# Performance work log

Measured on AMD Instinct MI355X. Metric: run time of the kernel, lower is better.

## Reference

```python
import jax, jax.numpy as jnp
import numpy as np

D_MODEL = 2048
HQ = 32          # query heads
HKV = 8          # kv heads
HD = D_MODEL // HQ   # head_dim = 64
G = HQ // HKV        # group size = 4
THETA = 10000.0


def _rope(x, pos):
    """x: (B, H, T, D), pos: (B, T) int. Rotates even/odd interleaved pairs."""
    D = x.shape[-1]
    inv_freq = THETA ** (-jnp.arange(0, D, 2, dtype=jnp.float32) / D)   # (D/2,)
    ang = pos[:, None, :, None].astype(jnp.float32) * inv_freq          # (B,1,T,D/2)
    cos, sin = jnp.cos(ang), jnp.sin(ang)
    x1, x2 = x[..., 0::2], x[..., 1::2]
    r1 = x1 * cos - x2 * sin
    r2 = x1 * sin + x2 * cos
    return jnp.stack([r1, r2], axis=-1).reshape(x.shape)


def setup_inputs() -> dict:
    key = jax.random.key(0)
    ks = jax.random.split(key, 5)
    B, T = 2, 2048
    s = lambda fan_in: 1.0 / np.sqrt(fan_in)
    return {
        "x": jax.random.normal(ks[0], (B, T, D_MODEL), jnp.float32),
        "token_positions": jnp.arange(T, dtype=jnp.int32),
        "WQ": jax.random.normal(ks[1], (HQ * HD, D_MODEL), jnp.float32) * s(D_MODEL),
        "WK": jax.random.normal(ks[2], (HKV * HD, D_MODEL), jnp.float32) * s(D_MODEL),
        "WV": jax.random.normal(ks[3], (HKV * HD, D_MODEL), jnp.float32) * s(D_MODEL),
        "WO": jax.random.normal(ks[4], (D_MODEL, HQ * HD), jnp.float32) * s(HQ * HD),
    }


def reference(x, token_positions, WQ, WK, WV, WO):
    B, T, _ = x.shape
    pos = token_positions if token_positions.ndim == 2 else jnp.broadcast_to(token_positions[None, :], (B, T))

    # Projections (Linear is y = x @ W.T, no bias)
    Q = (x @ WQ.T).reshape(B, T, HQ, HD).transpose(0, 2, 1, 3)    # (B,Hq,T,D)
    K = (x @ WK.T).reshape(B, T, HKV, HD).transpose(0, 2, 1, 3)   # (B,Hkv,T,D)
    V = (x @ WV.T).reshape(B, T, HKV, HD).transpose(0, 2, 1, 3)

    Q = _rope(Q, pos)
    K = _rope(K, pos)

    # GQA: group query heads per kv head instead of duplicating K/V
    Qg = Q.reshape(B, HKV, G, T, HD)
    scale = jnp.float32(1.0 / np.sqrt(HD))
    scores = jnp.einsum('bkgqd,bkld->bkgql', Qg, K) * scale       # (B,Hkv,G,T,T)

    causal = jnp.tril(jnp.ones((T, T), dtype=bool))
    scores = jnp.where(causal, scores, jnp.finfo(scores.dtype).min)
    A = jax.nn.softmax(scores, axis=-1)

    O = jnp.einsum('bkgql,bkld->bkgqd', A, V)                     # (B,Hkv,G,T,D)
    O = O.reshape(B, HQ, T, HD).transpose(0, 2, 1, 3).reshape(B, T, HQ * HD)
    return O @ WO.T
```

## Files before the change

### kernel.cpp

```cpp
#include <hip/hip_runtime.h>
#include <hip/hip_bf16.h>

#define B_   2
#define T_   2048
#define DM_  2048
#define HQ_  32
#define HKV_ 8
#define HD_  64

typedef __attribute__((ext_vector_type(8))) short bf16x8;
typedef __attribute__((ext_vector_type(4))) float f32x4;
typedef __fp16 f16x4 __attribute__((ext_vector_type(4)));
typedef __fp16 f16x2 __attribute__((ext_vector_type(2)));

__device__ __forceinline__ unsigned short f2bf(float f) {
    unsigned int u = __float_as_uint(f);
    u = (u + 0x7fffu + ((u >> 16) & 1u)) >> 16;
    return (unsigned short)u;
}

__device__ __forceinline__ void gload16(const unsigned short* g, unsigned short* l) {
    __builtin_amdgcn_global_load_lds(
        (const __attribute__((address_space(1))) unsigned int*)g,
        (__attribute__((address_space(3))) unsigned int*)l, 16, 0, 0);
}


__global__ __launch_bounds__(256) void convert_all(
    const float* __restrict__ x,  const float* __restrict__ WQ,
    const float* __restrict__ WK, const float* __restrict__ WV,
    const float* __restrict__ WO, unsigned short* __restrict__ ws)
{
    int i = blockIdx.x*256 + threadIdx.x;
    const float* src; unsigned short* dst; int rel;
    if (i < 2097152)      { src = x;  dst = ws;                 rel = i; }
    else if (i < 3145728) { src = WQ; dst = ws + 8388608;       rel = i - 2097152; }
    else if (i < 3407872) { src = WK; dst = ws + 8388608+4194304; rel = i - 3145728; }
    else if (i < 3670016) { src = WV; dst = ws + 8388608+5242880; rel = i - 3407872; }
    else                  { src = WO; dst = ws + 14680064;      rel = i - 3670016; }
    float4 v = *(const float4*)(src + (size_t)rel*4);
    uint2 pk;
    pk.x = (unsigned int)f2bf(v.x) | ((unsigned int)f2bf(v.y) << 16);
    pk.y = (unsigned int)f2bf(v.z) | ((unsigned int)f2bf(v.w) << 16);
    *(uint2*)(dst + (size_t)rel*4) = pk;
}

__global__ __launch_bounds__(256) void qkv_gemm_bf16(
    const unsigned short* __restrict__ Ab, const unsigned short* __restrict__ Wb,
    unsigned short* __restrict__ Qb, unsigned short* __restrict__ Kb,
    unsigned short* __restrict__ Vt)
{
    __shared__ unsigned short As[3][128*32];
    __shared__ unsigned short Bs[3][128*32];
    const int tid  = threadIdx.x;
    const int ln   = tid & 63;
    const int wv   = tid >> 6;
    const int wm   = (wv >> 1) * 64;
    const int wn   = (wv & 1) * 64;
    const int col  = ln & 15;
    const int quad = ln >> 4;

    const int bid = blockIdx.x;
    const int swz = (bid & 7) * 96 + (bid >> 3);
    const int n0  = (swz % 24) * 128;
    const int m0  = (swz / 24) * 128;

    const int cg = ((tid & 3) ^ ((tid >> 3) & 3)) * 8;
    const unsigned short* aG = Ab + (size_t)(m0 + (tid>>2))*DM_ + cg;
    const unsigned short* bG = Wb + (size_t)(n0 + (tid>>2))*DM_ + cg;
    const int ck = (quad ^ ((col >> 1) & 3)) * 8;

    f32x4 acc[4][4];
    #pragma unroll
    for (int i=0;i<4;++i)
        #pragma unroll
        for (int j=0;j<4;++j) { acc[i][j][0]=0.f; acc[i][j][1]=0.f; acc[i][j][2]=0.f; acc[i][j][3]=0.f; }

    auto stage = [&](int buf, int k0) {
        unsigned short* aL = &As[buf][wv*512];
        unsigned short* bL = &Bs[buf][wv*512];
        gload16(aG + k0,                  aL);
        gload16(aG + (size_t)64*DM_ + k0, aL + 2048);
        gload16(bG + k0,                  bL);
        gload16(bG + (size_t)64*DM_ + k0, bL + 2048);
    };

    stage(0, 0);
    stage(1, 32);

    int kt = 0;
    for (int k0 = 0; k0 < DM_; k0 += 32, ++kt) {
        if (k0 + 32 < DM_) {
            asm volatile("s_waitcnt vmcnt(4)" ::: "memory");
        } else {
            asm volatile("s_waitcnt vmcnt(0)" ::: "memory");
        }
        __builtin_amdgcn_s_barrier();
        if (k0 + 64 < DM_) stage((kt+2)%3, k0 + 64);
        const unsigned short* Ac = As[kt%3];
        const unsigned short* Bc = Bs[kt%3];
        bf16x8 af[4], bfr[4];
        #pragma unroll
        for (int i=0;i<4;++i) {
            af[i]  = *(const bf16x8*)&Ac[(wm + i*16 + col)*32 + ck];
            bfr[i] = *(const bf16x8*)&Bc[(wn + i*16 + col)*32 + ck];
        }
        #pragma unroll
        for (int i=0;i<4;++i)
            #pragma unroll
            for (int j=0;j<4;++j)
                acc[i][j] = __builtin_amdgcn_mfma_f32_16x16x32_bf16(af[i], bfr[j], acc[i][j], 0, 0, 0);
    }

    const int b  = m0 >> 11;
    const int tb = m0 & 2047;
    #pragma unroll
    for (int j=0;j<4;++j) {
        const int n = n0 + wn + j*16 + col;
        #pragma unroll
        for (int i=0;i<4;++i) {
            const int t = tb + wm + i*16 + quad*4;
            if (n < 2048) {
                #pragma unroll
                for (int r=0;r<4;++r)
                    Qb[(((size_t)(b*HQ_ + (n>>6)))*T_ + t + r)*HD_ + (n&63)] = f2bf(acc[i][j][r]);
            } else if (n < 2560) {
                #pragma unroll
                for (int r=0;r<4;++r)
                    Kb[(((size_t)(b*HKV_ + ((n-2048)>>6)))*T_ + t + r)*HD_ + (n&63)] = f2bf(acc[i][j][r]);
            } else {
                unsigned short* vp = Vt + (((size_t)(b*HKV_ + ((n-2560)>>6)))*HD_ + (n&63))*T_ + t;
                union { f16x2 h; unsigned int u; } c0, c1;
                c0.h = __builtin_amdgcn_cvt_pkrtz(acc[i][j][0], acc[i][j][1]);
                c1.h = __builtin_amdgcn_cvt_pkrtz(acc[i][j][2], acc[i][j][3]);
                *(unsigned int*)(vp)     = c0.u;
                *(unsigned int*)(vp + 2) = c1.u;
            }
        }
    }
}

__global__ __launch_bounds__(256) void rope_inplace(
    unsigned short* __restrict__ Qb, unsigned short* __restrict__ Kb,
    const int* __restrict__ pos)
{
    const int NQ = B_*HQ_*T_*(HD_/2);
    const int NK = B_*HKV_*T_*(HD_/2);
    int idx = blockIdx.x*256 + threadIdx.x;
    unsigned short* base; float scale;
    int rem;
    if (idx < NQ) { base = Qb; rem = idx; scale = 0.18033688011112042f; }
    else { rem = idx - NQ; if (rem >= NK) return; base = Kb; scale = 1.0f; }
    const int i  = rem & 31;
    const int t  = (rem >> 5) & (T_ - 1);
    const int bh = rem >> 16;
    size_t off = (((size_t)bh)*T_ + t)*HD_ + (i<<1);
    unsigned int pk = *(unsigned int*)(base + off);
    float x1 = __uint_as_float((pk & 0xffffu) << 16);
    float x2 = __uint_as_float(pk & 0xffff0000u);
    float p = (float)pos[t];
    float inv = exp2f(-13.287712379549449f * ((float)(i<<1)) * (1.0f/64.0f));
    float ang = p * inv;
    float sn, cs;
    sincosf(ang, &sn, &cs);
    float r1 = (x1*cs - x2*sn) * scale;
    float r2 = (x1*sn + x2*cs) * scale;
    unsigned int out = (unsigned int)f2bf(r1) | ((unsigned int)f2bf(r2) << 16);
    *(unsigned int*)(base + off) = out;
}

__global__ __launch_bounds__(256, 2) void attn_mfma(
    const unsigned short* __restrict__ Qb, const unsigned short* __restrict__ Kb,
    const unsigned short* __restrict__ Vh, unsigned short* __restrict__ Ob)
{
    __shared__ unsigned short Ks[2][64*64];
    __shared__ unsigned short Vs[2][64*64];

    const int tid  = threadIdx.x;
    const int lane = tid & 63;
    const int wave = tid >> 6;
    const int q16  = lane & 15;
    const int quad = lane >> 4;
    const int bxi  = blockIdx.x;
    const int bh   = blockIdx.y;
    const int b    = bh >> 5;
    const int h    = bh & 31;
    const int kvh  = h >> 2;
    const int qa   = bxi;
    const int qbt  = 31 - bxi;
    const int qgA  = qa *64 + wave*16 + q16;
    const int qgB  = qbt*64 + wave*16 + q16;

    const unsigned short* kbase = Kb + ((size_t)(b*HKV_ + kvh))*T_*HD_;
    const unsigned short* vbase = Vh + ((size_t)(b*HKV_ + kvh))*(size_t)HD_*T_;

    const bf16x8 qA0 = *(const bf16x8*)(Qb + ((size_t)bh*T_ + qgA)*HD_ + quad*8);
    const bf16x8 qA1 = *(const bf16x8*)(Qb + ((size_t)bh*T_ + qgA)*HD_ + 32 + quad*8);
    const bf16x8 qB0 = *(const bf16x8*)(Qb + ((size_t)bh*T_ + qgB)*HD_ + quad*8);
    const bf16x8 qB1 = *(const bf16x8*)(Qb + ((size_t)bh*T_ + qgB)*HD_ + 32 + quad*8);

    f32x4 oA[4], oB[4];
    #pragma unroll
    for (int i=0;i<4;++i) {
        oA[i][0]=0.f; oA[i][1]=0.f; oA[i][2]=0.f; oA[i][3]=0.f;
        oB[i][0]=0.f; oB[i][1]=0.f; oB[i][2]=0.f; oB[i][3]=0.f;
    }
    float lA = 0.f, lB = 0.f;

    const int sr = tid >> 3;
    const int sj = tid & 7;
    const int sc = (sj ^ (sr & 7)) * 8;

    const int rk7 = q16 & 7;
    const int ck0 = (quad ^ rk7) * 8;
    const int ck1 = ((quad + 4) ^ rk7) * 8;

    auto smrow = [&](const f32x4 s, float& ps) -> f16x4 {
        float e0 = exp2f(s[0]), e1 = exp2f(s[1]);
        float e2 = exp2f(s[2]), e3 = exp2f(s[3]);
        ps += (e0+e1) + (e2+e3);
        union { f16x2 h[2]; f16x4 v; } c;
        c.h[0] = __builtin_amdgcn_cvt_pkrtz(e0, e1);
        c.h[1] = __builtin_amdgcn_cvt_pkrtz(e2, e3);
        return c.v;
    };

    uint4 kr0, kr1, vr0, vr1;
    kr0 = *(const uint4*)(kbase + (size_t)sr*HD_ + sj*8);
    kr1 = *(const uint4*)(kbase + (size_t)(sr+32)*HD_ + sj*8);
    vr0 = *(const uint4*)(vbase + (size_t)sr*T_ + sj*8);
    vr1 = *(const uint4*)(vbase + (size_t)(sr+32)*T_ + sj*8);
    *(uint4*)&Ks[0][sr*64 + sc]      = kr0;
    *(uint4*)&Ks[0][(sr+32)*64 + sc] = kr1;
    *(uint4*)&Vs[0][sr*64 + sc]      = vr0;
    *(uint4*)&Vs[0][(sr+32)*64 + sc] = vr1;
    kr0 = *(const uint4*)(kbase + (size_t)(64+sr)*HD_ + sj*8);
    kr1 = *(const uint4*)(kbase + (size_t)(64+sr+32)*HD_ + sj*8);
    vr0 = *(const uint4*)(vbase + (size_t)sr*T_ + 64 + sj*8);
    vr1 = *(const uint4*)(vbase + (size_t)(sr+32)*T_ + 64 + sj*8);
    __syncthreads();

    int cur = 0;

    for (int kt = 0; kt <= qa; ++kt) {
        const unsigned short* KsC = Ks[cur];
        const unsigned short* VsC = Vs[cur];
        const int nxt = cur ^ 1;

        f32x4 sB[4], sA[4];
        #pragma unroll
        for (int t=0;t<4;++t) {
            sB[t][0]=0.f; sB[t][1]=0.f; sB[t][2]=0.f; sB[t][3]=0.f;
            sA[t][0]=0.f; sA[t][1]=0.f; sA[t][2]=0.f; sA[t][3]=0.f;
        }
        f16x4 pfB[4];
        float psB = 0.f, psA = 0.f;

        __builtin_amdgcn_s_setprio(1);
        #pragma unroll
        for (int t = 0; t < 4; ++t) {
            const int rk = (t*16 + q16) * 64;
            bf16x8 a0 = *(const bf16x8*)&KsC[rk + ck0];
            bf16x8 a1 = *(const bf16x8*)&KsC[rk + ck1];
            sB[t] = __builtin_amdgcn_mfma_f32_16x16x32_bf16(a0, qB0, sB[t], 0, 0, 0);
            sB[t] = __builtin_amdgcn_mfma_f32_16x16x32_bf16(a1, qB1, sB[t], 0, 0, 0);
            sA[t] = __builtin_amdgcn_mfma_f32_16x16x32_bf16(a0, qA0, sA[t], 0, 0, 0);
            sA[t] = __builtin_amdgcn_mfma_f32_16x16x32_bf16(a1, qA1, sA[t], 0, 0, 0);
            if (t > 0) pfB[t-1] = smrow(sB[t-1], psB);
        }
        *(uint4*)&Ks[nxt][sr*64 + sc]      = kr0;
        *(uint4*)&Ks[nxt][(sr+32)*64 + sc] = kr1;
        *(uint4*)&Vs[nxt][sr*64 + sc]      = vr0;
        *(uint4*)&Vs[nxt][(sr+32)*64 + sc] = vr1;
        if (kt + 1 < qbt) {
            const int kn = (kt+2)*64;
            kr0 = *(const uint4*)(kbase + (size_t)(kn+sr)*HD_ + sj*8);
            kr1 = *(const uint4*)(kbase + (size_t)(kn+sr+32)*HD_ + sj*8);
            vr0 = *(const uint4*)(vbase + (size_t)sr*T_ + kn + sj*8);
            vr1 = *(const uint4*)(vbase + (size_t)(sr+32)*T_ + kn + sj*8);
        }
        pfB[3] = smrow(sB[3], psB);
        lB += psB;

        if (kt == qa) {
            #pragma unroll
            for (int t = 0; t < 4; ++t)
                #pragma unroll
                for (int r = 0; r < 4; ++r)
                    if (kt*64 + t*16 + quad*4 + r > qgA) sA[t][r] = -1e30f;
        }

        #pragma unroll
        for (int t = 0; t < 4; ++t) {
            const int cv = ((2*t + (quad>>1)) ^ rk7) * 8 + (quad&1)*4;
            f16x4 va[4];
            #pragma unroll
            for (int dt=0;dt<4;++dt)
                va[dt] = *(const f16x4*)&VsC[(dt*16 + q16)*64 + cv];
            #pragma unroll
            for (int dt=0;dt<4;++dt)
                oB[dt] = __builtin_amdgcn_mfma_f32_16x16x16f16(va[dt], pfB[t], oB[dt], 0, 0, 0);
            f16x4 pfA = smrow(sA[t], psA);
            #pragma unroll
            for (int dt=0;dt<4;++dt)
                oA[dt] = __builtin_amdgcn_mfma_f32_16x16x16f16(va[dt], pfA, oA[dt], 0, 0, 0);
        }
        lA += psA;
        __builtin_amdgcn_s_setprio(0);
        __syncthreads();
        cur ^= 1;
    }

    for (int kt = qa+1; kt <= qbt; ++kt) {
        const unsigned short* KsC = Ks[cur];
        const unsigned short* VsC = Vs[cur];
        const int nxt = cur ^ 1;

        f32x4 sB[4];
        #pragma unroll
        for (int t=0;t<4;++t) { sB[t][0]=0.f; sB[t][1]=0.f; sB[t][2]=0.f; sB[t][3]=0.f; }

        __builtin_amdgcn_s_setprio(1);
        #pragma unroll
        for (int t = 0; t < 4; ++t) {
            const int rk = (t*16 + q16) * 64;
            bf16x8 a0 = *(const bf16x8*)&KsC[rk + ck0];
            bf16x8 a1 = *(const bf16x8*)&KsC[rk + ck1];
            sB[t] = __builtin_amdgcn_mfma_f32_16x16x32_bf16(a0, qB0, sB[t], 0, 0, 0);
            sB[t] = __builtin_amdgcn_mfma_f32_16x16x32_bf16(a1, qB1, sB[t], 0, 0, 0);
        }
        if (kt < qbt) {
            *(uint4*)&Ks[nxt][sr*64 + sc]      = kr0;
            *(uint4*)&Ks[nxt][(sr+32)*64 + sc] = kr1;
            *(uint4*)&Vs[nxt][sr*64 + sc]      = vr0;
            *(uint4*)&Vs[nxt][(sr+32)*64 + sc] = vr1;
        }
        if (kt + 1 < qbt) {
            const int kn = (kt+2)*64;
            kr0 = *(const uint4*)(kbase + (size_t)(kn+sr)*HD_ + sj*8);
            kr1 = *(const uint4*)(kbase + (size_t)(kn+sr+32)*HD_ + sj*8);
            vr0 = *(const uint4*)(vbase + (size_t)sr*T_ + kn + sj*8);
            vr1 = *(const uint4*)(vbase + (size_t)(sr+32)*T_ + kn + sj*8);
        }
        if (kt == qbt) {
            #pragma unroll
            for (int t = 0; t < 4; ++t)
                #pragma unroll
                for (int r = 0; r < 4; ++r)
                    if (kt*64 + t*16 + quad*4 + r > qgB) sB[t][r] = -1e30f;
        }

        float psB = 0.f;
        #pragma unroll
        for (int t = 0; t < 4; ++t) {
            f16x4 pfB = smrow(sB[t], psB);
            const int cv = ((2*t + (quad>>1)) ^ rk7) * 8 + (quad&1)*4;
            #pragma unroll
            for (int dt=0;dt<4;++dt) {
                f16x4 va = *(const f16x4*)&VsC[(dt*16 + q16)*64 + cv];
                oB[dt] = __builtin_amdgcn_mfma_f32_16x16x16f16(va, pfB, oB[dt], 0, 0, 0);
            }
        }
        lB += psB;
        __builtin_amdgcn_s_setprio(0);
        __syncthreads();
        cur ^= 1;
    }

    lA += __shfl_xor(lA, 16); lA += __shfl_xor(lA, 32);
    lB += __shfl_xor(lB, 16); lB += __shfl_xor(lB, 32);
    const float rlA = 1.0f / lA;
    const float rlB = 1.0f / lB;
    unsigned short* opA = Ob + ((size_t)(b*T_ + qgA))*(HQ_*HD_) + h*HD_;
    unsigned short* opB = Ob + ((size_t)(b*T_ + qgB))*(HQ_*HD_) + h*HD_;
    #pragma unroll
    for (int dt = 0; dt < 4; ++dt) {
        uint2 pa, pb;
        pa.x = (unsigned int)f2bf(oA[dt][0]*rlA) | ((unsigned int)f2bf(oA[dt][1]*rlA) << 16);
        pa.y = (unsigned int)f2bf(oA[dt][2]*rlA) | ((unsigned int)f2bf(oA[dt][3]*rlA) << 16);
        pb.x = (unsigned int)f2bf(oB[dt][0]*rlB) | ((unsigned int)f2bf(oB[dt][1]*rlB) << 16);
        pb.y = (unsigned int)f2bf(oB[dt][2]*rlB) | ((unsigned int)f2bf(oB[dt][3]*rlB) << 16);
        *(uint2*)(opA + dt*16 + quad*4) = pa;
        *(uint2*)(opB + dt*16 + quad*4) = pb;
    }
}

__global__ __launch_bounds__(256) void out_gemm_bf16(
    const unsigned short* __restrict__ Ab, const unsigned short* __restrict__ Wb,
    float* __restrict__ C)
{
    __shared__ unsigned short As[3][128*32];
    __shared__ unsigned short Bs[3][128*32];
    const int tid  = threadIdx.x;
    const int ln   = tid & 63;
    const int wv   = tid >> 6;
    const int wm   = (wv >> 1) * 64;
    const int wn   = (wv & 1) * 64;
    const int col  = ln & 15;
    const int quad = ln >> 4;

    const int bid = blockIdx.x;
    const int swz = (bid & 7) * 64 + (bid >> 3);
    const int n0  = (swz & 15) * 128;
    const int m0  = (swz >> 4) * 128;

    const int cg = ((tid & 3) ^ ((tid >> 3) & 3)) * 8;
    const unsigned short* aG = Ab + (size_t)(m0 + (tid>>2))*DM_ + cg;
    const unsigned short* bG = Wb + (size_t)(n0 + (tid>>2))*DM_ + cg;
    const int ck = (quad ^ ((col >> 1) & 3)) * 8;

    f32x4 acc[4][4];
    #pragma unroll
    for (int i=0;i<4;++i)
        #pragma unroll
        for (int j=0;j<4;++j) { acc[i][j][0]=0.f; acc[i][j][1]=0.f; acc[i][j][2]=0.f; acc[i][j][3]=0.f; }

    auto stage = [&](int buf, int k0) {
        unsigned short* aL = &As[buf][wv*512];
        unsigned short* bL = &Bs[buf][wv*512];
        gload16(aG + k0,                  aL);
        gload16(aG + (size_t)64*DM_ + k0, aL + 2048);
        gload16(bG + k0,                  bL);
        gload16(bG + (size_t)64*DM_ + k0, bL + 2048);
    };

    stage(0, 0);
    stage(1, 32);

    int kt = 0;
    for (int k0 = 0; k0 < DM_; k0 += 32, ++kt) {
        if (k0 + 32 < DM_) {
            asm volatile("s_waitcnt vmcnt(4)" ::: "memory");
        } else {
            asm volatile("s_waitcnt vmcnt(0)" ::: "memory");
        }
        __builtin_amdgcn_s_barrier();
        if (k0 + 64 < DM_) stage((kt+2)%3, k0 + 64);
        const unsigned short* Ac = As[kt%3];
        const unsigned short* Bc = Bs[kt%3];
        bf16x8 af[4], bfr[4];
        #pragma unroll
        for (int i=0;i<4;++i) {
            af[i]  = *(const bf16x8*)&Ac[(wm + i*16 + col)*32 + ck];
            bfr[i] = *(const bf16x8*)&Bc[(wn + i*16 + col)*32 + ck];
        }
        #pragma unroll
        for (int i=0;i<4;++i)
            #pragma unroll
            for (int j=0;j<4;++j)
                acc[i][j] = __builtin_amdgcn_mfma_f32_16x16x32_bf16(af[i], bfr[j], acc[i][j], 0, 0, 0);
    }

    #pragma unroll
    for (int i=0;i<4;++i) {
        const int m = m0 + wm + i*16 + quad*4;
        #pragma unroll
        for (int j=0;j<4;++j) {
            const int n = n0 + wn + j*16 + col;
            #pragma unroll
            for (int r=0;r<4;++r)
                C[(size_t)(m + r)*DM_ + n] = acc[i][j][r];
        }
    }
}

extern "C" void kernel_launch(void* const* d_in, const int* in_sizes, int n_in,
                              void* d_out, int out_size, void* d_ws, size_t ws_size,
                              hipStream_t stream) {
    const float* x   = (const float*)d_in[0];
    const int*   pos = (const int*)  d_in[1];
    const float* WQ  = (const float*)d_in[2];
    const float* WK  = (const float*)d_in[3];
    const float* WV  = (const float*)d_in[4];
    const float* WO  = (const float*)d_in[5];
    float* out = (float*)d_out;

    unsigned short* xb  = (unsigned short*)d_ws;
    unsigned short* Wb  = xb  + (size_t)8388608;
    unsigned short* WOb = Wb  + (size_t)6291456;
    unsigned short* Qb  = WOb + (size_t)4194304;
    unsigned short* Kb  = Qb  + (size_t)8388608;
    unsigned short* Vt  = Kb  + (size_t)2097152;
    unsigned short* Ob  = Vt  + (size_t)2097152;

    convert_all<<<18432, 256, 0, stream>>>(x, WQ, WK, WV, WO, (unsigned short*)d_ws);

    qkv_gemm_bf16<<<768, 256, 0, stream>>>(xb, Wb, Qb, Kb, Vt);

    const int pairs = B_*HQ_*T_*(HD_/2) + B_*HKV_*T_*(HD_/2);
    rope_inplace<<<(pairs + 255)/256, 256, 0, stream>>>(Qb, Kb, pos);

    dim3 g3(16, B_*HQ_);
    attn_mfma<<<g3, 256, 0, stream>>>(Qb, Kb, Vt, Ob);

    out_gemm_bf16<<<512, 256, 0, stream>>>(Ob, WOb, out);
}
```

Measured before the change: 333.1 us.

## Fuse RoPE into QKV GEMM epilogue with precomputed trig table

```diff
diff --git a/kernel.cpp b/kernel.cpp
--- a/kernel.cpp
+++ b/kernel.cpp
@@ -26,12 +26,27 @@
 }
 
 
+#define CONV_N 4718592
+
 __global__ __launch_bounds__(256) void convert_all(
     const float* __restrict__ x,  const float* __restrict__ WQ,
     const float* __restrict__ WK, const float* __restrict__ WV,
-    const float* __restrict__ WO, unsigned short* __restrict__ ws)
+    const float* __restrict__ WO, unsigned short* __restrict__ ws,
+    const int* __restrict__ pos,  float* __restrict__ trig)
 {
     int i = blockIdx.x*256 + threadIdx.x;
+    if (i >= CONV_N) {
+        int j = i - CONV_N;
+        if (j < T_*32) {
+            int t = j >> 5, p = j & 31;
+            float inv = exp2f(-0.4152410118609203f * (float)p);
+            float ang = (float)pos[t] * inv;
+            float sn, cs;
+            sincosf(ang, &sn, &cs);
+            *(float2*)&trig[j*2] = make_float2(cs, sn);
+        }
+        return;
+    }
     const float* src; unsigned short* dst; int rel;
     if (i < 2097152)      { src = x;  dst = ws;                 rel = i; }
     else if (i < 3145728) { src = WQ; dst = ws + 8388608;       rel = i - 2097152; }
@@ -48,7 +63,7 @@
 __global__ __launch_bounds__(256) void qkv_gemm_bf16(
     const unsigned short* __restrict__ Ab, const unsigned short* __restrict__ Wb,
     unsigned short* __restrict__ Qb, unsigned short* __restrict__ Kb,
-    unsigned short* __restrict__ Vt)
+    unsigned short* __restrict__ Vt, const float* __restrict__ trig)
 {
     __shared__ unsigned short As[3][128*32];
     __shared__ unsigned short Bs[3][128*32];
@@ -85,50 +100,75 @@
         gload16(bG + (size_t)64*DM_ + k0, bL + 2048);
     };
 
+    auto kstep = [&](int bc, int k0v, int bstage, bool dostage, bool last) {
+        if (last) asm volatile("s_waitcnt vmcnt(0)" ::: "memory");
+        else      asm volatile("s_waitcnt vmcnt(4)" ::: "memory");
+        __builtin_amdgcn_s_barrier();
+        if (dostage) stage(bstage, k0v + 64);
+        const unsigned short* Ac = As[bc];
+        const unsigned short* Bc = Bs[bc];
+        bf16x8 af[4], bfr[4];
+        #pragma unroll
+        for (int i2=0;i2<4;++i2) {
+            af[i2]  = *(const bf16x8*)&Ac[(wm + i2*16 + col)*32 + ck];
+            bfr[i2] = *(const bf16x8*)&Bc[(wn + i2*16 + col)*32 + ck];
+        }
+        #pragma unroll
+        for (int i2=0;i2<4;++i2)
+            #pragma unroll
+            for (int j2=0;j2<4;++j2)
+                acc[i2][j2] = __builtin_amdgcn_mfma_f32_16x16x32_bf16(af[i2], bfr[j2], acc[i2][j2], 0, 0, 0);
+    };
+
     stage(0, 0);
     stage(1, 32);
 
-    int kt = 0;
-    for (int k0 = 0; k0 < DM_; k0 += 32, ++kt) {
-        if (k0 + 32 < DM_) {
-            asm volatile("s_waitcnt vmcnt(4)" ::: "memory");
-        } else {
-            asm volatile("s_waitcnt vmcnt(0)" ::: "memory");
-        }
-        __builtin_amdgcn_s_barrier();
-        if (k0 + 64 < DM_) stage((kt+2)%3, k0 + 64);
-        const unsigned short* Ac = As[kt%3];
-        const unsigned short* Bc = Bs[kt%3];
-        bf16x8 af[4], bfr[4];
-        #pragma unroll
-        for (int i=0;i<4;++i) {
-            af[i]  = *(const bf16x8*)&Ac[(wm + i*16 + col)*32 + ck];
-            bfr[i] = *(const bf16x8*)&Bc[(wn + i*16 + col)*32 + ck];
-        }
-        #pragma unroll
-        for (int i=0;i<4;++i)
-            #pragma unroll
-            for (int j=0;j<4;++j)
-                acc[i][j] = __builtin_amdgcn_mfma_f32_16x16x32_bf16(af[i], bfr[j], acc[i][j], 0, 0, 0);
-    }
+    int k0 = 0;
+    for (int rep = 0; rep < 20; ++rep) {
+        kstep(0, k0,      2, true, false);
+        kstep(1, k0+32,   0, true, false);
+        kstep(2, k0+64,   1, true, false);
+        k0 += 96;
+    }
+    kstep(0, 1920, 2, true,  false);
+    kstep(1, 1952, 0, true,  false);
+    kstep(2, 1984, 1, false, false);
+    kstep(0, 2016, 0, false, true);
 
     const int b  = m0 >> 11;
     const int tb = m0 & 2047;
     #pragma unroll
     for (int j=0;j<4;++j) {
         const int n = n0 + wn + j*16 + col;
-        #pragma unroll
-        for (int i=0;i<4;++i) {
-            const int t = tb + wm + i*16 + quad*4;
-            if (n < 2048) {
+        if (n < 2560) {
+            const int d   = n & 63;
+            const int p   = d >> 1;
+            const bool ev = (d & 1) == 0;
+            const float sc = (n < 2048) ? 0.18033688011112042f : 1.0f;
+            unsigned short* outp = (n < 2048)
+                ? Qb + (((size_t)(b*HQ_  + (n>>6)))*T_)*HD_
+                : Kb + (((size_t)(b*HKV_ + ((n-2048)>>6)))*T_)*HD_;
+            #pragma unroll
+            for (int i=0;i<4;++i) {
+                const int t0 = tb + wm + i*16 + quad*4;
                 #pragma unroll
-                for (int r=0;r<4;++r)
-                    Qb[(((size_t)(b*HQ_ + (n>>6)))*T_ + t + r)*HD_ + (n&63)] = f2bf(acc[i][j][r]);
-            } else if (n < 2560) {
-                #pragma unroll
-                for (int r=0;r<4;++r)
-                    Kb[(((size_t)(b*HKV_ + ((n-2048)>>6)))*T_ + t + r)*HD_ + (n&63)] = f2bf(acc[i][j][r]);
-            } else {
+                for (int r=0;r<4;++r) {
+                    float self = acc[i][j][r];
+                    float part = __shfl_xor(self, 1);
+                    float2 cs  = *(const float2*)&trig[((t0 + r)*32 + p)*2];
+                    float out  = ev ? (self*cs.x - part*cs.y)
+                                    : (part*cs.y + self*cs.x);
+                    out *= sc;
+                    unsigned int pk = (unsigned int)f2bf(out);
+                    unsigned int po = __shfl_xor(pk, 1);
+                    if (ev)
+                        *(unsigned int*)(outp + (size_t)(t0 + r)*HD_ + d) = pk | (po << 16);
+                }
+            }
+        } else {
+            #pragma unroll
+            for (int i=0;i<4;++i) {
+                const int t = tb + wm + i*16 + quad*4;
                 unsigned short* vp = Vt + (((size_t)(b*HKV_ + ((n-2560)>>6)))*HD_ + (n&63))*T_ + t;
                 union { f16x2 h; unsigned int u; } c0, c1;
                 c0.h = __builtin_amdgcn_cvt_pkrtz(acc[i][j][0], acc[i][j][1]);
@@ -138,35 +178,6 @@
             }
         }
     }
-}
-
-__global__ __launch_bounds__(256) void rope_inplace(
-    unsigned short* __restrict__ Qb, unsigned short* __restrict__ Kb,
-    const int* __restrict__ pos)
-{
-    const int NQ = B_*HQ_*T_*(HD_/2);
-    const int NK = B_*HKV_*T_*(HD_/2);
-    int idx = blockIdx.x*256 + threadIdx.x;
-    unsigned short* base; float scale;
-    int rem;
-    if (idx < NQ) { base = Qb; rem = idx; scale = 0.18033688011112042f; }
-    else { rem = idx - NQ; if (rem >= NK) return; base = Kb; scale = 1.0f; }
-    const int i  = rem & 31;
-    const int t  = (rem >> 5) & (T_ - 1);
-    const int bh = rem >> 16;
-    size_t off = (((size_t)bh)*T_ + t)*HD_ + (i<<1);
-    unsigned int pk = *(unsigned int*)(base + off);
-    float x1 = __uint_as_float((pk & 0xffffu) << 16);
-    float x2 = __uint_as_float(pk & 0xffff0000u);
-    float p = (float)pos[t];
-    float inv = exp2f(-13.287712379549449f * ((float)(i<<1)) * (1.0f/64.0f));
-    float ang = p * inv;
-    float sn, cs;
-    sincosf(ang, &sn, &cs);
-    float r1 = (x1*cs - x2*sn) * scale;
-    float r2 = (x1*sn + x2*cs) * scale;
-    unsigned int out = (unsigned int)f2bf(r1) | ((unsigned int)f2bf(r2) << 16);
-    *(unsigned int*)(base + off) = out;
 }
 
 __global__ __launch_bounds__(256, 2) void attn_mfma(
@@ -424,32 +435,40 @@
         gload16(bG + (size_t)64*DM_ + k0, bL + 2048);
     };
 
+    auto kstep = [&](int bc, int k0v, int bstage, bool dostage, bool last) {
+        if (last) asm volatile("s_waitcnt vmcnt(0)" ::: "memory");
+        else      asm volatile("s_waitcnt vmcnt(4)" ::: "memory");
+        __builtin_amdgcn_s_barrier();
+        if (dostage) stage(bstage, k0v + 64);
+        const unsigned short* Ac = As[bc];
+        const unsigned short* Bc = Bs[bc];
+        bf16x8 af[4], bfr[4];
+        #pragma unroll
+        for (int i2=0;i2<4;++i2) {
+            af[i2]  = *(const bf16x8*)&Ac[(wm + i2*16 + col)*32 + ck];
+            bfr[i2] = *(const bf16x8*)&Bc[(wn + i2*16 + col)*32 + ck];
+        }
+        #pragma unroll
+        for (int i2=0;i2<4;++i2)
+            #pragma unroll
+            for (int j2=0;j2<4;++j2)
+                acc[i2][j2] = __builtin_amdgcn_mfma_f32_16x16x32_bf16(af[i2], bfr[j2], acc[i2][j2], 0, 0, 0);
+    };
+
     stage(0, 0);
     stage(1, 32);
 
-    int kt = 0;
-    for (int k0 = 0; k0 < DM_; k0 += 32, ++kt) {
-        if (k0 + 32 < DM_) {
-            asm volatile("s_waitcnt vmcnt(4)" ::: "memory");
-        } else {
-            asm volatile("s_waitcnt vmcnt(0)" ::: "memory");
-        }
-        __builtin_amdgcn_s_barrier();
-        if (k0 + 64 < DM_) stage((kt+2)%3, k0 + 64);
-        const unsigned short* Ac = As[kt%3];
-        const unsigned short* Bc = Bs[kt%3];
-        bf16x8 af[4], bfr[4];
-        #pragma unroll
-        for (int i=0;i<4;++i) {
-            af[i]  = *(const bf16x8*)&Ac[(wm + i*16 + col)*32 + ck];
-            bfr[i] = *(const bf16x8*)&Bc[(wn + i*16 + col)*32 + ck];
-        }
-        #pragma unroll
-        for (int i=0;i<4;++i)
-            #pragma unroll
-            for (int j=0;j<4;++j)
-                acc[i][j] = __builtin_amdgcn_mfma_f32_16x16x32_bf16(af[i], bfr[j], acc[i][j], 0, 0, 0);
-    }
+    int k0 = 0;
+    for (int rep = 0; rep < 20; ++rep) {
+        kstep(0, k0,      2, true, false);
+        kstep(1, k0+32,   0, true, false);
+        kstep(2, k0+64,   1, true, false);
+        k0 += 96;
+    }
+    kstep(0, 1920, 2, true,  false);
+    kstep(1, 1952, 0, true,  false);
+    kstep(2, 1984, 1, false, false);
+    kstep(0, 2016, 0, false, true);
 
     #pragma unroll
     for (int i=0;i<4;++i) {
@@ -482,13 +501,11 @@
     unsigned short* Kb  = Qb  + (size_t)8388608;
     unsigned short* Vt  = Kb  + (size_t)2097152;
     unsigned short* Ob  = Vt  + (size_t)2097152;
-
-    convert_all<<<18432, 256, 0, stream>>>(x, WQ, WK, WV, WO, (unsigned short*)d_ws);
-
-    qkv_gemm_bf16<<<768, 256, 0, stream>>>(xb, Wb, Qb, Kb, Vt);
-
-    const int pairs = B_*HQ_*T_*(HD_/2) + B_*HKV_*T_*(HD_/2);
-    rope_inplace<<<(pairs + 255)/256, 256, 0, stream>>>(Qb, Kb, pos);
+    float* trig = (float*)Ob;
+
+    convert_all<<<18688, 256, 0, stream>>>(x, WQ, WK, WV, WO, (unsigned short*)d_ws, pos, trig);
+
+    qkv_gemm_bf16<<<768, 256, 0, stream>>>(xb, Wb, Qb, Kb, Vt, trig);
 
     dim3 g3(16, B_*HQ_);
     attn_mfma<<<g3, 256, 0, stream>>>(Qb, Kb, Vt, Ob);
```

After: 302.7 us. 1.1x faster.
